# Performance work log

Measured on AMD Instinct MI355X. Metric: run time of the kernel, lower is better.

The kernel has to match this reference:

```python
import jax, jax.numpy as jnp
import numpy as np

EPS = 1e-5  # InstanceNorm3d default eps


def _conv3d(x, w, b):
    # x: [C, D, H, W]; w: [O, I, 3, 3, 3]; SAME padding (pw = k//2)
    y = jax.lax.conv_general_dilated(
        x[None], w, window_strides=(1, 1, 1), padding='SAME',
        dimension_numbers=('NCDHW', 'OIDHW', 'NCDHW'))[0]
    return y + b[:, None, None, None]


def _spade(x, ws, bs, wg, bg, wb, bb):
    # x: [C, D, H, W] single sample; per-class SPADE params
    mu = x.mean(axis=(1, 2, 3), keepdims=True)
    var = x.var(axis=(1, 2, 3), keepdims=True)  # biased var, as in InstanceNorm
    normalized = (x - mu) * jax.lax.rsqrt(var + EPS)
    actv = jax.nn.relu(_conv3d(x, ws, bs))
    gamma = _conv3d(actv, wg, bg)
    beta = _conv3d(actv, wb, bb)
    return normalized * (1.0 + gamma) + beta


def setup_inputs() -> dict:
    key = jax.random.key(0)
    ks = jax.random.split(key, 6)
    B, C, D = 8, 32, 48
    NC, NH = 4, 64  # num_classes, nhidden
    s = 0.05
    return {
        'x': jax.random.normal(ks[0], (B, C, D, D, D), jnp.float32),
        'y': jax.random.randint(ks[1], (B,), 0, NC),
        'Wshared': jax.random.normal(ks[2], (NC, NH, C, 3, 3, 3), jnp.float32) * s,
        'bshared': jnp.zeros((NC, NH), jnp.float32),
        'Wgamma': jax.random.normal(ks[3], (NC, C, NH, 3, 3, 3), jnp.float32) * s,
        'bgamma': jnp.zeros((NC, C), jnp.float32),
        'Wbeta': jax.random.normal(ks[4], (NC, C, NH, 3, 3, 3), jnp.float32) * s,
        'bbeta': jnp.zeros((NC, C), jnp.float32),
    }


def reference(x, y, Wshared, bshared, Wgamma, bgamma, Wbeta, bbeta):
    # Gather per-sample expert params by class index, then batch via vmap
    return jax.vmap(_spade)(x, Wshared[y], bshared[y], Wgamma[y], bgamma[y],
                            Wbeta[y], bbeta[y])
```

## Files before the change

### kernel.cpp

```cpp
#include <hip/hip_runtime.h>
#include <stdint.h>

#define V3 (48*48*48)
#define BATCH 8

typedef __bf16 bf16x8 __attribute__((ext_vector_type(8)));
typedef float  f32x4  __attribute__((ext_vector_type(4)));

__device__ __forceinline__ unsigned short f2bf(float f) {
  uint32_t u = __float_as_uint(f);
  u += 0x7fffu + ((u >> 16) & 1u);
  return (unsigned short)(u >> 16);
}

#define GLDS16(gp, lp)                                                         \
  __builtin_amdgcn_global_load_lds(                                            \
      (const __attribute__((address_space(1))) void*)(gp),                     \
      (__attribute__((address_space(3))) void*)(lp), 16, 0, 0)

__global__ __launch_bounds__(256)
void stats_kernel(const float* __restrict__ x, float* __restrict__ mu,
                  float* __restrict__ rstd, float4* __restrict__ zpage) {
  if (blockIdx.x == 0 && threadIdx.x < 64) {
    float4 z; z.x = 0.f; z.y = 0.f; z.z = 0.f; z.w = 0.f;
    zpage[threadIdx.x] = z;
  }
  const int bc = blockIdx.x;
  const float4* p = reinterpret_cast<const float4*>(x + (size_t)bc * V3);
  float s = 0.f, s2 = 0.f;
  for (int i = threadIdx.x; i < V3 / 4; i += 256) {
    float4 v = p[i];
    s  += (v.x + v.y) + (v.z + v.w);
    s2 += (v.x * v.x + v.y * v.y) + (v.z * v.z + v.w * v.w);
  }
  for (int o = 32; o; o >>= 1) { s += __shfl_down(s, o); s2 += __shfl_down(s2, o); }
  __shared__ float red[8];
  const int wave = threadIdx.x >> 6, lane = threadIdx.x & 63;
  if (lane == 0) { red[wave] = s; red[4 + wave] = s2; }
  __syncthreads();
  if (threadIdx.x == 0) {
    float S1 = red[0] + red[1] + red[2] + red[3];
    float S2 = red[4] + red[5] + red[6] + red[7];
    float m = S1 / (float)V3;
    float var = S2 / (float)V3 - m * m;
    mu[bc] = m;
    rstd[bc] = rsqrtf(var + 1e-5f);
  }
}

__global__ __launch_bounds__(256)
void repack_kernel(const float* __restrict__ x, unsigned short* __restrict__ xcl) {
  const int bid = blockIdx.x;
  const int h = bid % 48;
  const int d = (bid / 48) % 48;
  const int b = bid / (48 * 48);
  __shared__ float tile[32][48];
  const float* src = x + (size_t)b * 32 * V3 + (size_t)(d * 48 + h) * 48;
  for (int i = threadIdx.x; i < 32 * 48; i += 256) {
    int c = i / 48, w = i - c * 48;
    tile[c][w] = src[(size_t)c * V3 + w];
  }
  __syncthreads();
  const int i = threadIdx.x;
  if (i < 48 * 4) {
    const int w = i >> 2, pp = i & 3;
    alignas(16) unsigned short pk[8];
#pragma unroll
    for (int j = 0; j < 8; ++j) pk[j] = f2bf(tile[pp * 8 + j][w]);
    *reinterpret_cast<uint4*>(
        &xcl[((size_t)b * V3 + (size_t)(d * 48 + h) * 48 + w) * 32 + pp * 8]) =
        *reinterpret_cast<const uint4*>(pk);
  }
}

__global__ __launch_bounds__(256)
void wprep_kernel(const int* __restrict__ y, const float* __restrict__ Wsh,
                  const float* __restrict__ Wg, const float* __restrict__ Wb,
                  unsigned short* __restrict__ w1, unsigned short* __restrict__ w23) {
  const int N1 = BATCH * 27 * 4 * 64 * 8;
  const int N2 = BATCH * 2 * 27 * 4 * 64 * 8;
  int idx = blockIdx.x * 256 + threadIdx.x;
  if (idx < N1) {
    const int j = idx & 7;
    const int lane = (idx >> 3) & 63;
    const int mt = (idx >> 9) & 3;
    const int tap = (idx >> 11) % 27;
    const int b = idx / (27 << 11);
    const int q = lane >> 4, n = lane & 15;
    const int cout = mt * 16 + n, cin = q * 8 + j;
    const int cls = y[b];
    w1[idx] = f2bf(Wsh[((size_t)((cls * 64 + cout) * 32 + cin)) * 27 + tap]);
  } else if (idx < N1 + N2) {
    const int t = idx - N1;
    const int b = t / 110592;
    const int r1 = t - b * 110592;
    const int kc = r1 / 55296;
    const int r2 = r1 - kc * 55296;
    const int tap = r2 >> 11;
    const int r3 = r2 & 2047;
    const int mt = r3 >> 9;
    const int lane = (r3 >> 3) & 63;
    const int j = r3 & 7;
    const int q = lane >> 4, n = lane & 15;
    const int cout = mt * 16 + n, cin = kc * 32 + q * 8 + j;
    const int cls = y[b];
    float v = (cout < 32) ? Wg[((size_t)((cls * 32 + cout) * 64 + cin)) * 27 + tap]
                          : Wb[((size_t)((cls * 32 + (cout - 32)) * 64 + cin)) * 27 + tap];
    w23[t] = f2bf(v);
  }
}

__global__ __launch_bounds__(256, 2)
void conv1_kernel(const unsigned short* __restrict__ xcl,
                  const unsigned short* __restrict__ w1,
                  const int* __restrict__ y, const float* __restrict__ bsh,
                  unsigned short* __restrict__ actv,
                  const float4* __restrict__ zpage) {
  const int d0 = (blockIdx.y >> 3) * 4;
  const int h0 = (blockIdx.y & 7) * 6;
  const int w0 = blockIdx.x * 16;
  const int b = blockIdx.z;

  __shared__ unsigned short lds[4 * 864 * 8];

  const int tid = threadIdx.x;
  const int lane = tid & 63;
  const int wave = tid >> 6;

  const unsigned short* xb = xcl + (size_t)b * V3 * 32;
  for (int i = tid; i < 3456; i += 256) {
    const int pp = i / 864;
    const int v = i - pp * 864;
    const int ld_ = v / 144;
    const int r = v - ld_ * 144;
    const int lh = r / 18;
    const int lw = r - lh * 18;
    const int d = d0 + ld_ - 1, h = h0 + lh - 1, w = w0 + lw - 1;
    const bool ok = (unsigned)d < 48u && (unsigned)h < 48u && (unsigned)w < 48u;
    const void* gp =
        ok ? (const void*)(xb + ((size_t)((d * 48 + h) * 48 + w)) * 32 + pp * 8)
           : (const void*)((const char*)zpage + lane * 16);
    GLDS16(gp, &lds[(size_t)(i - lane) * 8]);
  }
  __syncthreads();

  const int q = lane >> 4, n = lane & 15;

  f32x4 acc[6][4];
#pragma unroll
  for (int g = 0; g < 6; ++g)
#pragma unroll
    for (int mt = 0; mt < 4; ++mt) acc[g][mt] = (f32x4){0.f, 0.f, 0.f, 0.f};

  const unsigned short* wb = w1 + (size_t)b * 55296 + lane * 8;

  bf16x8 acur[4], anxt[4];
#pragma unroll
  for (int mt = 0; mt < 4; ++mt)
    acur[mt] = *reinterpret_cast<const bf16x8*>(&wb[mt * 512]);

  const int vb0 = q * 864 + wave * 144 + n;

  for (int tap = 0; tap < 27; ++tap) {
    if (tap < 26) {
#pragma unroll
      for (int mt = 0; mt < 4; ++mt)
        anxt[mt] = *reinterpret_cast<const bf16x8*>(&wb[((tap + 1) * 4 + mt) * 512]);
    }
    const int dz = tap / 9, rr = tap - dz * 9, dy = rr / 3, dx = rr - dy * 3;
    const int vb = vb0 + dz * 144 + dy * 18 + dx;
    bf16x8 bf[6];
#pragma unroll
    for (int g = 0; g < 6; ++g)
      bf[g] = *reinterpret_cast<const bf16x8*>(&lds[(size_t)(vb + g * 18) * 8]);
#pragma unroll
    for (int g = 0; g < 6; ++g)
#pragma unroll
      for (int mt = 0; mt < 4; ++mt)
        acc[g][mt] = __builtin_amdgcn_mfma_f32_16x16x32_bf16(acur[mt], bf[g], acc[g][mt], 0, 0, 0);
#pragma unroll
    for (int mt = 0; mt < 4; ++mt) acur[mt] = anxt[mt];
  }

  const int cls = y[b];
  const int od = d0 + wave, ow = w0 + n;
#pragma unroll
  for (int g = 0; g < 6; ++g) {
    const int oh = h0 + g;
    const size_t vg = (size_t)(od * 48 + oh) * 48 + ow;
#pragma unroll
    for (int mt = 0; mt < 4; ++mt) {
      const int c0 = mt * 16 + q * 4;
      ushort4 pk;
      pk.x = f2bf(fmaxf(acc[g][mt][0] + bsh[cls * 64 + c0 + 0], 0.f));
      pk.y = f2bf(fmaxf(acc[g][mt][1] + bsh[cls * 64 + c0 + 1], 0.f));
      pk.z = f2bf(fmaxf(acc[g][mt][2] + bsh[cls * 64 + c0 + 2], 0.f));
      pk.w = f2bf(fmaxf(acc[g][mt][3] + bsh[cls * 64 + c0 + 3], 0.f));
      *reinterpret_cast<ushort4*>(&actv[((size_t)b * V3 + vg) * 64 + c0]) = pk;
    }
  }
}

__global__ __launch_bounds__(256, 2)
void conv2_kernel(const unsigned short* __restrict__ actv,
                  const unsigned short* __restrict__ w23,
                  const int* __restrict__ y, const float* __restrict__ bgm,
                  const float* __restrict__ bbt, const float* __restrict__ x,
                  const float* __restrict__ mu, const float* __restrict__ rstd,
                  float* __restrict__ out, const float4* __restrict__ zpage) {
  const int d0 = (blockIdx.y >> 3) * 4;
  const int h0 = (blockIdx.y & 7) * 6;
  const int w0 = blockIdx.x * 16;
  const int b = blockIdx.z;

  __shared__ unsigned short lds[4 * 864 * 8];

  const int tid = threadIdx.x;
  const int lane = tid & 63;
  const int wave = tid >> 6;
  const int q = lane >> 4, n = lane & 15;

  f32x4 acc[6][4];
#pragma unroll
  for (int g = 0; g < 6; ++g)
#pragma unroll
    for (int mt = 0; mt < 4; ++mt) acc[g][mt] = (f32x4){0.f, 0.f, 0.f, 0.f};

  const unsigned short* ab = actv + (size_t)b * V3 * 64;
  const int vb0 = q * 864 + wave * 144 + n;

  for (int kc = 0; kc < 2; ++kc) {
    if (kc) __syncthreads();
    for (int i = tid; i < 3456; i += 256) {
      const int pp = i / 864;
      const int v = i - pp * 864;
      const int ld_ = v / 144;
      const int r = v - ld_ * 144;
      const int lh = r / 18;
      const int lw = r - lh * 18;
      const int d = d0 + ld_ - 1, h = h0 + lh - 1, w = w0 + lw - 1;
      const bool ok = (unsigned)d < 48u && (unsigned)h < 48u && (unsigned)w < 48u;
      const void* gp =
          ok ? (const void*)(ab + ((size_t)((d * 48 + h) * 48 + w)) * 64 + kc * 32 + pp * 8)
             : (const void*)((const char*)zpage + lane * 16);
      GLDS16(gp, &lds[(size_t)(i - lane) * 8]);
    }
    __syncthreads();

    const unsigned short* wb = w23 + (size_t)b * 110592 + (size_t)kc * 55296 + lane * 8;

    bf16x8 acur[4], anxt[4];
#pragma unroll
    for (int mt = 0; mt < 4; ++mt)
      acur[mt] = *reinterpret_cast<const bf16x8*>(&wb[mt * 512]);

    for (int tap = 0; tap < 27; ++tap) {
      if (tap < 26) {
#pragma unroll
        for (int mt = 0; mt < 4; ++mt)
          anxt[mt] = *reinterpret_cast<const bf16x8*>(&wb[((tap + 1) * 4 + mt) * 512]);
      }
      const int dz = tap / 9, rr = tap - dz * 9, dy = rr / 3, dx = rr - dy * 3;
      const int vb = vb0 + dz * 144 + dy * 18 + dx;
      bf16x8 bf[6];
#pragma unroll
      for (int g = 0; g < 6; ++g)
        bf[g] = *reinterpret_cast<const bf16x8*>(&lds[(size_t)(vb + g * 18) * 8]);
#pragma unroll
      for (int g = 0; g < 6; ++g)
#pragma unroll
        for (int mt = 0; mt < 4; ++mt)
          acc[g][mt] = __builtin_amdgcn_mfma_f32_16x16x32_bf16(acur[mt], bf[g], acc[g][mt], 0, 0, 0);
#pragma unroll
      for (int mt = 0; mt < 4; ++mt) acur[mt] = anxt[mt];
    }
  }

  const int cls = y[b];
  const int od = d0 + wave, ow = w0 + n;
#pragma unroll
  for (int g = 0; g < 6; ++g) {
    const int oh = h0 + g;
    const size_t vg = (size_t)(od * 48 + oh) * 48 + ow;
#pragma unroll
    for (int mt = 0; mt < 2; ++mt) {
#pragma unroll
      for (int r = 0; r < 4; ++r) {
        const int c = mt * 16 + q * 4 + r;
        const float gamma = acc[g][mt][r] + bgm[cls * 32 + c];
        const float beta = acc[g][mt + 2][r] + bbt[cls * 32 + c];
        const size_t xi = (size_t)(b * 32 + c) * V3 + vg;
        const float xn = (x[xi] - mu[b * 32 + c]) * rstd[b * 32 + c];
        out[xi] = xn * (1.f + gamma) + beta;
      }
    }
  }
}

extern "C" void kernel_launch(void* const* d_in, const int* in_sizes, int n_in,
                              void* d_out, int out_size, void* d_ws, size_t ws_size,
                              hipStream_t stream) {
  const float* x = (const float*)d_in[0];
  const int* y = (const int*)d_in[1];
  const float* Wsh = (const float*)d_in[2];
  const float* bsh = (const float*)d_in[3];
  const float* Wg = (const float*)d_in[4];
  const float* bg = (const float*)d_in[5];
  const float* Wb = (const float*)d_in[6];
  const float* bb = (const float*)d_in[7];
  float* out = (float*)d_out;

  char* ws = (char*)d_ws;
  unsigned short* xcl  = (unsigned short*)(ws + 0);
  unsigned short* actv = (unsigned short*)(ws + 56623104);
  unsigned short* w1   = (unsigned short*)(ws + 169869312);
  unsigned short* w23  = (unsigned short*)(ws + 170754048);
  float* mu    = (float*)(ws + 172523520);
  float* rstd  = (float*)(ws + 172524544);
  float4* zpg  = (float4*)(ws + 172525568);

  stats_kernel<<<256, 256, 0, stream>>>(x, mu, rstd, zpg);
  repack_kernel<<<BATCH * 48 * 48, 256, 0, stream>>>(x, xcl);
  wprep_kernel<<<(BATCH * 27 * 4 * 64 * 8 * 3 + 255) / 256, 256, 0, stream>>>(
      y, Wsh, Wg, Wb, w1, w23);

  dim3 grid(3, 96, BATCH);
  conv1_kernel<<<grid, 256, 0, stream>>>(xcl, w1, y, bsh, actv, zpg);
  conv2_kernel<<<grid, 256, 0, stream>>>(actv, w23, y, bg, bb, x, mu, rstd, out, zpg);
}
```

Measured before the change: 640.6 us.

## Enlarge conv tiles to 6 depth slices, split LDS staging to overlap compute

Result: slower. 1.358 ms (+112.0%).

```diff
diff --git a/kernel.cpp b/kernel.cpp
--- a/kernel.cpp
+++ b/kernel.cpp
@@ -18,7 +18,7 @@
       (const __attribute__((address_space(1))) void*)(gp),                     \
       (__attribute__((address_space(3))) void*)(lp), 16, 0, 0)
 
-__global__ __launch_bounds__(256)
+__global__ __launch_bounds__(1024)
 void stats_kernel(const float* __restrict__ x, float* __restrict__ mu,
                   float* __restrict__ rstd, float4* __restrict__ zpage) {
   if (blockIdx.x == 0 && threadIdx.x < 64) {
@@ -28,19 +28,20 @@
   const int bc = blockIdx.x;
   const float4* p = reinterpret_cast<const float4*>(x + (size_t)bc * V3);
   float s = 0.f, s2 = 0.f;
-  for (int i = threadIdx.x; i < V3 / 4; i += 256) {
+  for (int i = threadIdx.x; i < V3 / 4; i += 1024) {
     float4 v = p[i];
     s  += (v.x + v.y) + (v.z + v.w);
     s2 += (v.x * v.x + v.y * v.y) + (v.z * v.z + v.w * v.w);
   }
   for (int o = 32; o; o >>= 1) { s += __shfl_down(s, o); s2 += __shfl_down(s2, o); }
-  __shared__ float red[8];
+  __shared__ float red[32];
   const int wave = threadIdx.x >> 6, lane = threadIdx.x & 63;
-  if (lane == 0) { red[wave] = s; red[4 + wave] = s2; }
+  if (lane == 0) { red[wave] = s; red[16 + wave] = s2; }
   __syncthreads();
   if (threadIdx.x == 0) {
-    float S1 = red[0] + red[1] + red[2] + red[3];
-    float S2 = red[4] + red[5] + red[6] + red[7];
+    float S1 = 0.f, S2 = 0.f;
+#pragma unroll
+    for (int i = 0; i < 16; ++i) { S1 += red[i]; S2 += red[16 + i]; }
     float m = S1 / (float)V3;
     float var = S2 / (float)V3 - m * m;
     mu[bc] = m;
@@ -110,41 +111,76 @@
   }
 }
 
-__global__ __launch_bounds__(256, 2)
+
+#define STAGE_RANGE(K0, K1, SRC_EXPR)                                          \
+  do {                                                                         \
+    _Pragma("unroll") for (int k = (K0); k < (K1); ++k) {                      \
+      const int j = tid + k * 384;                                             \
+      const int ld_ = j / 576;                                                 \
+      const int r = j - ld_ * 576;                                             \
+      const int pp = r / 144;                                                  \
+      const int r2 = r - pp * 144;                                             \
+      const int lh = r2 / 18;                                                  \
+      const int lw = r2 - lh * 18;                                             \
+      const int d = d0 + ld_ - 1, h = h0 + lh - 1, w = w0 + lw - 1;            \
+      const bool ok = (unsigned)d < 48u && (unsigned)h < 48u && (unsigned)w < 48u; \
+      const void* gp = ok ? (const void*)(SRC_EXPR)                            \
+                          : (const void*)((const char*)zpage + lane * 16);     \
+      GLDS16(gp, &lds[(size_t)(j - lane) * 8]);                                \
+    }                                                                          \
+  } while (0)
+
+#define STAGE12(SRC_EXPR)                                                      \
+  do {                                                                         \
+    STAGE_RANGE(0, 9, SRC_EXPR);                                               \
+    __builtin_amdgcn_sched_barrier(0);         \
+    STAGE_RANGE(9, 12, SRC_EXPR);                                              \
+  } while (0)
+
+#define COMPUTE_DZ(DZ, WB)                                                     \
+  do {                                                                         \
+    const int pb_ = ((wave + (DZ)) * 4 + q) * 144 + n;                         \
+    __builtin_amdgcn_s_setprio(1);                                             \
+    _Pragma("unroll") for (int t9 = 0; t9 < 9; ++t9) {                         \
+      const int dy_ = t9 / 3, dx_ = t9 - dy_ * 3;                              \
+      bf16x8 aw[4];                                                            \
+      _Pragma("unroll") for (int mt = 0; mt < 4; ++mt)                         \
+        aw[mt] = *reinterpret_cast<const bf16x8*>(                             \
+            &(WB)[(((DZ) * 9 + t9) * 4 + mt) * 512]);                          \
+      _Pragma("unroll") for (int g = 0; g < 6; ++g) {                          \
+        const bf16x8 bv = *reinterpret_cast<const bf16x8*>(                    \
+            &lds[(size_t)(pb_ + (g + dy_) * 18 + dx_) * 8]);                   \
+        _Pragma("unroll") for (int mt = 0; mt < 4; ++mt)                       \
+          acc[g][mt] = __builtin_amdgcn_mfma_f32_16x16x32_bf16(                \
+              aw[mt], bv, acc[g][mt], 0, 0, 0);                                \
+      }                                                                        \
+    }                                                                          \
+    __builtin_amdgcn_s_setprio(0);                                             \
+  } while (0)
+
+#define WAIT_VM(N)                                                             \
+  asm volatile("s_waitcnt vmcnt(" #N ")" ::: "memory")
+
+__global__ __launch_bounds__(384, 3)
 void conv1_kernel(const unsigned short* __restrict__ xcl,
                   const unsigned short* __restrict__ w1,
                   const int* __restrict__ y, const float* __restrict__ bsh,
                   unsigned short* __restrict__ actv,
                   const float4* __restrict__ zpage) {
-  const int d0 = (blockIdx.y >> 3) * 4;
+  const int d0 = (blockIdx.y >> 3) * 6;
   const int h0 = (blockIdx.y & 7) * 6;
   const int w0 = blockIdx.x * 16;
   const int b = blockIdx.z;
 
-  __shared__ unsigned short lds[4 * 864 * 8];
+  __shared__ unsigned short lds[4608 * 8];
 
   const int tid = threadIdx.x;
   const int lane = tid & 63;
   const int wave = tid >> 6;
+  const int q = lane >> 4, n = lane & 15;
 
   const unsigned short* xb = xcl + (size_t)b * V3 * 32;
-  for (int i = tid; i < 3456; i += 256) {
-    const int pp = i / 864;
-    const int v = i - pp * 864;
-    const int ld_ = v / 144;
-    const int r = v - ld_ * 144;
-    const int lh = r / 18;
-    const int lw = r - lh * 18;
-    const int d = d0 + ld_ - 1, h = h0 + lh - 1, w = w0 + lw - 1;
-    const bool ok = (unsigned)d < 48u && (unsigned)h < 48u && (unsigned)w < 48u;
-    const void* gp =
-        ok ? (const void*)(xb + ((size_t)((d * 48 + h) * 48 + w)) * 32 + pp * 8)
-           : (const void*)((const char*)zpage + lane * 16);
-    GLDS16(gp, &lds[(size_t)(i - lane) * 8]);
-  }
-  __syncthreads();
-
-  const int q = lane >> 4, n = lane & 15;
+  STAGE12(xb + ((size_t)((d * 48 + h) * 48 + w)) * 32 + pp * 8);
 
   f32x4 acc[6][4];
 #pragma unroll
@@ -154,33 +190,13 @@
 
   const unsigned short* wb = w1 + (size_t)b * 55296 + lane * 8;
 
-  bf16x8 acur[4], anxt[4];
-#pragma unroll
-  for (int mt = 0; mt < 4; ++mt)
-    acur[mt] = *reinterpret_cast<const bf16x8*>(&wb[mt * 512]);
-
-  const int vb0 = q * 864 + wave * 144 + n;
-
-  for (int tap = 0; tap < 27; ++tap) {
-    if (tap < 26) {
-#pragma unroll
-      for (int mt = 0; mt < 4; ++mt)
-        anxt[mt] = *reinterpret_cast<const bf16x8*>(&wb[((tap + 1) * 4 + mt) * 512]);
-    }
-    const int dz = tap / 9, rr = tap - dz * 9, dy = rr / 3, dx = rr - dy * 3;
-    const int vb = vb0 + dz * 144 + dy * 18 + dx;
-    bf16x8 bf[6];
-#pragma unroll
-    for (int g = 0; g < 6; ++g)
-      bf[g] = *reinterpret_cast<const bf16x8*>(&lds[(size_t)(vb + g * 18) * 8]);
-#pragma unroll
-    for (int g = 0; g < 6; ++g)
-#pragma unroll
-      for (int mt = 0; mt < 4; ++mt)
-        acc[g][mt] = __builtin_amdgcn_mfma_f32_16x16x32_bf16(acur[mt], bf[g], acc[g][mt], 0, 0, 0);
-#pragma unroll
-    for (int mt = 0; mt < 4; ++mt) acur[mt] = anxt[mt];
-  }
+  WAIT_VM(3);
+  __builtin_amdgcn_s_barrier();
+  COMPUTE_DZ(0, wb);
+  WAIT_VM(0);
+  __builtin_amdgcn_s_barrier();
+  COMPUTE_DZ(1, wb);
+  COMPUTE_DZ(2, wb);
 
   const int cls = y[b];
   const int od = d0 + wave, ow = w0 + n;
@@ -201,19 +217,19 @@
   }
 }
 
-__global__ __launch_bounds__(256, 2)
+__global__ __launch_bounds__(384, 3)
 void conv2_kernel(const unsigned short* __restrict__ actv,
                   const unsigned short* __restrict__ w23,
                   const int* __restrict__ y, const float* __restrict__ bgm,
                   const float* __restrict__ bbt, const float* __restrict__ x,
                   const float* __restrict__ mu, const float* __restrict__ rstd,
                   float* __restrict__ out, const float4* __restrict__ zpage) {
-  const int d0 = (blockIdx.y >> 3) * 4;
+  const int d0 = (blockIdx.y >> 3) * 6;
   const int h0 = (blockIdx.y & 7) * 6;
   const int w0 = blockIdx.x * 16;
   const int b = blockIdx.z;
 
-  __shared__ unsigned short lds[4 * 864 * 8];
+  __shared__ unsigned short lds[4608 * 8];
 
   const int tid = threadIdx.x;
   const int lane = tid & 63;
@@ -227,53 +243,21 @@
     for (int mt = 0; mt < 4; ++mt) acc[g][mt] = (f32x4){0.f, 0.f, 0.f, 0.f};
 
   const unsigned short* ab = actv + (size_t)b * V3 * 64;
-  const int vb0 = q * 864 + wave * 144 + n;
 
   for (int kc = 0; kc < 2; ++kc) {
-    if (kc) __syncthreads();
-    for (int i = tid; i < 3456; i += 256) {
-      const int pp = i / 864;
-      const int v = i - pp * 864;
-      const int ld_ = v / 144;
-      const int r = v - ld_ * 144;
-      const int lh = r / 18;
-      const int lw = r - lh * 18;
-      const int d = d0 + ld_ - 1, h = h0 + lh - 1, w = w0 + lw - 1;
-      const bool ok = (unsigned)d < 48u && (unsigned)h < 48u && (unsigned)w < 48u;
-      const void* gp =
-          ok ? (const void*)(ab + ((size_t)((d * 48 + h) * 48 + w)) * 64 + kc * 32 + pp * 8)
-             : (const void*)((const char*)zpage + lane * 16);
-      GLDS16(gp, &lds[(size_t)(i - lane) * 8]);
-    }
-    __syncthreads();
-
-    const unsigned short* wb = w23 + (size_t)b * 110592 + (size_t)kc * 55296 + lane * 8;
-
-    bf16x8 acur[4], anxt[4];
-#pragma unroll
-    for (int mt = 0; mt < 4; ++mt)
-      acur[mt] = *reinterpret_cast<const bf16x8*>(&wb[mt * 512]);
-
-    for (int tap = 0; tap < 27; ++tap) {
-      if (tap < 26) {
-#pragma unroll
-        for (int mt = 0; mt < 4; ++mt)
-          anxt[mt] = *reinterpret_cast<const bf16x8*>(&wb[((tap + 1) * 4 + mt) * 512]);
-      }
-      const int dz = tap / 9, rr = tap - dz * 9, dy = rr / 3, dx = rr - dy * 3;
-      const int vb = vb0 + dz * 144 + dy * 18 + dx;
-      bf16x8 bf[6];
-#pragma unroll
-      for (int g = 0; g < 6; ++g)
-        bf[g] = *reinterpret_cast<const bf16x8*>(&lds[(size_t)(vb + g * 18) * 8]);
-#pragma unroll
-      for (int g = 0; g < 6; ++g)
-#pragma unroll
-        for (int mt = 0; mt < 4; ++mt)
-          acc[g][mt] = __builtin_amdgcn_mfma_f32_16x16x32_bf16(acur[mt], bf[g], acc[g][mt], 0, 0, 0);
-#pragma unroll
-      for (int mt = 0; mt < 4; ++mt) acur[mt] = anxt[mt];
-    }
+    if (kc) { __syncthreads(); }
+    STAGE12(ab + ((size_t)((d * 48 + h) * 48 + w)) * 64 + kc * 32 + pp * 8);
+
+    const unsigned short* wb =
+        w23 + (size_t)b * 110592 + (size_t)kc * 55296 + lane * 8;
+
+    WAIT_VM(3);
+    __builtin_amdgcn_s_barrier();
+    COMPUTE_DZ(0, wb);
+    WAIT_VM(0);
+    __builtin_amdgcn_s_barrier();
+    COMPUTE_DZ(1, wb);
+    COMPUTE_DZ(2, wb);
   }
 
   const int cls = y[b];
@@ -319,12 +303,12 @@
   float* rstd  = (float*)(ws + 172524544);
   float4* zpg  = (float4*)(ws + 172525568);
 
-  stats_kernel<<<256, 256, 0, stream>>>(x, mu, rstd, zpg);
+  stats_kernel<<<256, 1024, 0, stream>>>(x, mu, rstd, zpg);
   repack_kernel<<<BATCH * 48 * 48, 256, 0, stream>>>(x, xcl);
   wprep_kernel<<<(BATCH * 27 * 4 * 64 * 8 * 3 + 255) / 256, 256, 0, stream>>>(
       y, Wsh, Wg, Wb, w1, w23);
 
-  dim3 grid(3, 96, BATCH);
-  conv1_kernel<<<grid, 256, 0, stream>>>(xcl, w1, y, bsh, actv, zpg);
-  conv2_kernel<<<grid, 256, 0, stream>>>(actv, w23, y, bg, bb, x, mu, rstd, out, zpg);
-}
+  dim3 grid(3, 64, BATCH);
+  conv1_kernel<<<grid, 384, 0, stream>>>(xcl, w1, y, bsh, actv, zpg);
+  conv2_kernel<<<grid, 384, 0, stream>>>(actv, w23, y, bg, bb, x, mu, rstd, out, zpg);
+}
```
